# Kernel tuning notes

Hardware: AMD Instinct MI355X
Metric: run time of the kernel (lower is better)

## Reference

```python
import math
import jax, jax.numpy as jnp
import numpy as np

B, N, C = 2, 2048, 768
H, DH = 12, 64  # num_heads, head_dim


def setup_inputs() -> dict:
    key = jax.random.key(0)
    ks = jax.random.split(key, 5)
    s = 1.0 / math.sqrt(C)  # keep linear outputs O(1)
    return {
        "x": jax.random.normal(ks[0], (B, N, C), jnp.float32),
        "Wq": jax.random.normal(ks[1], (C, C), jnp.float32) * s,
        "bq": jnp.zeros((C,), jnp.float32),
        "Wk": jax.random.normal(ks[2], (C, C), jnp.float32) * s,
        "bk": jnp.zeros((C,), jnp.float32),
        "Wv": jax.random.normal(ks[3], (C, C), jnp.float32) * s,
        "bv": jnp.zeros((C,), jnp.float32),
        "Wp": jax.random.normal(ks[4], (C, C), jnp.float32) * s,
        "bp": jnp.zeros((C,), jnp.float32),
    }


def reference(x, Wq, bq, Wk, bk, Wv, bv, Wp, bp):
    # Linear projections; torch nn.Linear computes x @ W.T + b, here W stored
    # as (in, out) so it's x @ W + b with equivalent math.
    def split(t):  # [B,N,C] -> [B,H,N,DH]
        return t.reshape(B, N, H, DH).transpose(0, 2, 1, 3)

    q = split(x @ Wq + bq)
    k = split(x @ Wk + bk)
    v = split(x @ Wv + bv)
    scale = 1.0 / math.sqrt(DH)
    attn = jnp.einsum("bhqd,bhkd->bhqk", q, k) * scale  # [B,H,N,N]
    attn = jax.nn.softmax(attn, axis=-1)  # attn_drop=0.0 -> identity
    y = jnp.einsum("bhqk,bhkd->bhqd", attn, v)  # [B,H,N,DH]
    y = y.transpose(0, 2, 1, 3).reshape(B, N, C)
    return y @ Wp + bp  # proj_drop=0.0 -> identity
```

## Files before the change

### kernel.cpp

```cpp
#include <hip/hip_runtime.h>


typedef __bf16 bf16_t;
typedef __bf16 bf16x8 __attribute__((ext_vector_type(8)));
typedef __bf16 bf16x4 __attribute__((ext_vector_type(4)));
typedef short  short4_t __attribute__((ext_vector_type(4)));
typedef float  floatx4 __attribute__((ext_vector_type(4)));

#define MFMA32(a, b, c) __builtin_amdgcn_mfma_f32_16x16x32_bf16(a, b, c, 0, 0, 0)
#define MFMA16(a, b, c) __builtin_amdgcn_mfma_f32_16x16x16bf16_1k(a, b, c, 0, 0, 0)

__device__ __forceinline__ void gload16(const bf16_t* g, bf16_t* l) {
  __builtin_amdgcn_global_load_lds(
      (__attribute__((address_space(1))) void*)g,
      (__attribute__((address_space(3))) void*)l, 16, 0, 0);
}

__global__ __launch_bounds__(256) void cvt_all_kernel(
    const float* __restrict__ x, const float* __restrict__ W0,
    const float* __restrict__ W1, const float* __restrict__ W2,
    const float* __restrict__ W3, bf16_t* __restrict__ xb,
    bf16_t* __restrict__ T0, bf16_t* __restrict__ T1,
    bf16_t* __restrict__ T2, bf16_t* __restrict__ T3) {
  __shared__ bf16_t T[64][65];
  const int id = blockIdx.x;
  if (id < 3072) {
    int i = id * 256 + threadIdx.x;
    floatx4 v = ((const floatx4*)x)[i];
    bf16x4 o;
    o[0] = (bf16_t)v[0]; o[1] = (bf16_t)v[1]; o[2] = (bf16_t)v[2]; o[3] = (bf16_t)v[3];
    ((bf16x4*)xb)[i] = o;
    return;
  }
  const int wid = id - 3072;
  const int z = wid / 144, rem = wid % 144;
  const int by = rem / 12, bx = rem % 12;
  const float* W = (z == 0) ? W0 : (z == 1) ? W1 : (z == 2) ? W2 : W3;
  bf16_t* WT = (z == 0) ? T0 : (z == 1) ? T1 : (z == 2) ? T2 : T3;
  const int c = threadIdx.x & 63, r0 = threadIdx.x >> 6;
  const int i0 = by * 64, o0 = bx * 64;
#pragma unroll
  for (int p = 0; p < 16; ++p) {
    int r = p * 4 + r0;
    T[r][c] = (bf16_t)W[(i0 + r) * 768 + o0 + c];
  }
  __syncthreads();
#pragma unroll
  for (int p = 0; p < 16; ++p) {
    int r = p * 4 + r0;
    WT[(o0 + r) * 768 + i0 + c] = T[c][r];
  }
}

#define LDPG 72


#define LOADSET(KT)                                        \
  sa0 = *(const bf16x8*)(gA + (KT));                       \
  sa1 = *(const bf16x8*)(gA + (KT) + 32 * 768);            \
  sa2 = *(const bf16x8*)(gA + (KT) + 64 * 768);            \
  sa3 = *(const bf16x8*)(gA + (KT) + 96 * 768);            \
  sb0 = *(const bf16x8*)(gB + (KT));                       \
  sb1 = *(const bf16x8*)(gB + (KT) + 32 * 768);            \
  sb2 = *(const bf16x8*)(gB + (KT) + 64 * 768);            \
  sb3 = *(const bf16x8*)(gB + (KT) + 96 * 768);

#define WRITESET(LA, LB)                                   \
  *(bf16x8*)(LA) = sa0;                                    \
  *(bf16x8*)((LA) + 32 * LDPG) = sa1;                      \
  *(bf16x8*)((LA) + 64 * LDPG) = sa2;                      \
  *(bf16x8*)((LA) + 96 * LDPG) = sa3;                      \
  *(bf16x8*)(LB) = sb0;                                    \
  *(bf16x8*)((LB) + 32 * LDPG) = sb1;                      \
  *(bf16x8*)((LB) + 64 * LDPG) = sb2;                      \
  *(bf16x8*)((LB) + 96 * LDPG) = sb3;

#define GCOMPUTE(BUF)                                                       \
  {                                                                         \
    _Pragma("unroll") for (int kk2 = 0; kk2 < 2; ++kk2) {                   \
      bf16x8 af[4], bfr[4];                                                 \
      _Pragma("unroll") for (int i = 0; i < 4; ++i) {                       \
        af[i]  = *(bf16x8*)&Al[BUF][(wr * 64 + i * 16 + l15) * LDPG +       \
                                    kk2 * 32 + quad * 8];                   \
        bfr[i] = *(bf16x8*)&Bl[BUF][(wc * 64 + i * 16 + l15) * LDPG +       \
                                    kk2 * 32 + quad * 8];                   \
      }                                                                     \
      _Pragma("unroll") for (int mi = 0; mi < 4; ++mi)                      \
          _Pragma("unroll") for (int ni = 0; ni < 4; ++ni)                  \
              acc[mi][ni] = MFMA32(af[mi], bfr[ni], acc[mi][ni]);           \
    }                                                                       \
  }

#define GEMM_KLOOP()                                       \
  LOADSET(0);                                              \
  WRITESET(lA0, lB0);                                      \
  LOADSET(64);                                             \
  __syncthreads();                                         \
  for (int t = 0; t < 12; t += 2) {                        \
    GCOMPUTE(0);                                           \
    WRITESET(lA1, lB1);                      \
    if (t + 2 < 12) LOADSET((t + 2) * 64);                 \
    __syncthreads();                                       \
    GCOMPUTE(1);                                           \
    if (t + 2 < 12) {                                      \
      WRITESET(lA0, lB0);                    \
      if (t + 3 < 12) LOADSET((t + 3) * 64);               \
    }                                                      \
    __syncthreads();                                       \
  }

__global__ __launch_bounds__(256, 2) void gemm_qkv(
    const bf16_t* __restrict__ Xb, const bf16_t* __restrict__ WqT,
    const bf16_t* __restrict__ WkT, const bf16_t* __restrict__ WvT,
    const float* __restrict__ bq, const float* __restrict__ bk,
    const float* __restrict__ bv, bf16_t* __restrict__ qw,
    bf16_t* __restrict__ kw, bf16_t* __restrict__ vtw) {
  __shared__ bf16_t Al[2][128 * LDPG];
  __shared__ bf16_t Bl[2][128 * LDPG];
  const int z = blockIdx.z;
  const bf16_t* Wt = (z == 0) ? WqT : (z == 1) ? WkT : WvT;
  const float* bias = (z == 0) ? bq : (z == 1) ? bk : bv;
  const float oscale = (z == 0) ? 0.18033688011112042f : 1.0f;

  const int tid = threadIdx.x, lane = tid & 63, w = tid >> 6;
  const int wr = w >> 1, wc = w & 1;
  const int l15 = lane & 15, quad = lane >> 4;
  const int m0 = blockIdx.y * 128, n0 = blockIdx.x * 128;

  const int r0 = tid >> 3, q0c = (tid & 7) * 8;
  const bf16_t* gA = &Wt[(m0 + r0) * 768 + q0c];
  const bf16_t* gB = &Xb[(n0 + r0) * 768 + q0c];
  bf16_t* lA0 = &Al[0][r0 * LDPG + q0c];
  bf16_t* lB0 = &Bl[0][r0 * LDPG + q0c];
  bf16_t* lA1 = &Al[1][r0 * LDPG + q0c];
  bf16_t* lB1 = &Bl[1][r0 * LDPG + q0c];

  floatx4 acc[4][4] = {};
  bf16x8 sa0, sa1, sa2, sa3, sb0, sb1, sb2, sb3;

  GEMM_KLOOP();

  const int hh = (m0 + wr * 64) >> 6;
#pragma unroll
  for (int mi = 0; mi < 4; ++mi) {
    const int d0 = mi * 16 + quad * 4;
    const int gm0 = m0 + wr * 64 + d0;
    float bv4[4];
#pragma unroll
    for (int r = 0; r < 4; ++r) bv4[r] = bias[gm0 + r];
#pragma unroll
    for (int ni = 0; ni < 4; ++ni) {
      const int gn = n0 + wc * 64 + ni * 16 + l15;
      const int bb = gn >> 11, tok = gn & 2047;
      const int bh = bb * 12 + hh;
      if (z == 0) {
        bf16x4 pk;
#pragma unroll
        for (int r = 0; r < 4; ++r)
          pk[r] = (bf16_t)((acc[mi][ni][r] + bv4[r]) * oscale);
        *(bf16x4*)&qw[bh * 131072 + tok * 64 + d0] = pk;
      } else if (z == 1) {
        const int kt2 = tok >> 7, k128 = tok & 127;
        const int nk = k128 >> 4, kl15 = k128 & 15;
        const int kk = d0 >> 5, kq = (d0 >> 3) & 3, j0 = d0 & 7;
        bf16x4 pk;
#pragma unroll
        for (int r = 0; r < 4; ++r)
          pk[r] = (bf16_t)(acc[mi][ni][r] + bv4[r]);
        *(bf16x4*)&kw[bh * 131072 + kt2 * 8192 +
                      ((nk * 2 + kk) * 64 + kq * 16 + kl15) * 8 + j0] = pk;
      } else {
        const int kt2 = tok >> 7, k128 = tok & 127;
        const int nk = k128 >> 4, vq = (k128 >> 2) & 3, j = k128 & 3;
        const int nd = d0 >> 4, vl0 = d0 & 15;
        const int base = bh * 131072 + kt2 * 8192 +
                         ((nk * 4 + nd) * 64 + vq * 16 + vl0) * 4 + j;
#pragma unroll
        for (int r = 0; r < 4; ++r)
          vtw[base + r * 4] = (bf16_t)(acc[mi][ni][r] + bv4[r]);
      }
    }
  }
}

__global__ __launch_bounds__(256, 2) void gemm_proj(
    const bf16_t* __restrict__ Yb, const bf16_t* __restrict__ WpT,
    const float* __restrict__ bias, float* __restrict__ out) {
  __shared__ bf16_t Al[2][128 * LDPG];
  __shared__ bf16_t Bl[2][128 * LDPG];
  const int tid = threadIdx.x, lane = tid & 63, w = tid >> 6;
  const int wr = w >> 1, wc = w & 1;
  const int l15 = lane & 15, quad = lane >> 4;
  const int m0 = blockIdx.y * 128, n0 = blockIdx.x * 128;

  const int r0 = tid >> 3, q0c = (tid & 7) * 8;
  const bf16_t* gA = &WpT[(m0 + r0) * 768 + q0c];
  const bf16_t* gB = &Yb[(n0 + r0) * 768 + q0c];
  bf16_t* lA0 = &Al[0][r0 * LDPG + q0c];
  bf16_t* lB0 = &Bl[0][r0 * LDPG + q0c];
  bf16_t* lA1 = &Al[1][r0 * LDPG + q0c];
  bf16_t* lB1 = &Bl[1][r0 * LDPG + q0c];

  floatx4 acc[4][4] = {};
  bf16x8 sa0, sa1, sa2, sa3, sb0, sb1, sb2, sb3;

  GEMM_KLOOP();

#pragma unroll
  for (int mi = 0; mi < 4; ++mi) {
    const int gm0 = m0 + wr * 64 + mi * 16 + quad * 4;
    floatx4 bv4;
#pragma unroll
    for (int r = 0; r < 4; ++r) bv4[r] = bias[gm0 + r];
#pragma unroll
    for (int ni = 0; ni < 4; ++ni) {
      const int gn = n0 + wc * 64 + ni * 16 + l15;
      floatx4 v = acc[mi][ni] + bv4;
      *(floatx4*)&out[gn * 768 + gm0] = v;
    }
  }
}

__global__ __launch_bounds__(256, 4) void attn_kernel(
    const bf16_t* __restrict__ Q, const bf16_t* __restrict__ Kf,
    const bf16_t* __restrict__ Vf, bf16_t* __restrict__ Y) {
  __shared__ __align__(16) bf16_t smem[16384];
  __shared__ float Ls[2][2][2][16];
  float* Ox = (float*)smem;

  const int tid = threadIdx.x, lane = tid & 63, w = tid >> 6;
  const int wq = w & 1, wk = w >> 1;
  const int l15 = lane & 15, quad = lane >> 4;

  const int i = blockIdx.x;
  const int xcd = i & 7, j = i >> 3;
  const int bh = xcd * 3 + (j >> 5);
  const int q0 = (j & 31) * 64;

  const bf16_t* Qb = Q + bh * 131072;
  const bf16_t* Kg = Kf + bh * 131072 + tid * 8;
  const bf16_t* Vg = Vf + bh * 131072 + tid * 8;

  bf16x8 qf[2][2];
#pragma unroll
  for (int ni = 0; ni < 2; ++ni)
#pragma unroll
    for (int kk = 0; kk < 2; ++kk)
      qf[ni][kk] = *(const bf16x8*)&Qb[(q0 + wq * 32 + ni * 16 + l15) * 64 +
                                       kk * 32 + quad * 8];

  floatx4 oacc[2][4] = {};
  floatx4 sacc[2] = {};
  const short4_t ones = {0x3F80, 0x3F80, 0x3F80, 0x3F80};

  auto stage = [&](int b, int t) {
    const bf16_t* kg = Kg + t * 4096;
    const bf16_t* vg = Vg + t * 4096;
    bf16_t* kl = smem + b * 8192 + tid * 8;
    bf16_t* vl = smem + b * 8192 + 4096 + tid * 8;
    gload16(kg, kl);
    gload16(kg + 2048, kl + 2048);
    gload16(vg, vl);
    gload16(vg + 2048, vl + 2048);
  };

  auto compute = [&](int b) {
    const bf16_t* Kl = smem + b * 8192;
    const bf16_t* Vl = smem + b * 8192 + 4096;
    short4_t pk[2][2];
#pragma unroll
    for (int mt = 0; mt < 2; ++mt) {
      floatx4 s[2] = {};
#pragma unroll
      for (int kk = 0; kk < 2; ++kk) {
        bf16x8 kfr = *(const bf16x8*)&Kl[((wk * 2 + mt) * 2 + kk) * 512 + lane * 8];
#pragma unroll
        for (int ni = 0; ni < 2; ++ni)
          s[ni] = MFMA32(kfr, qf[ni][kk], s[ni]);
      }
#pragma unroll
      for (int ni = 0; ni < 2; ++ni) {
        bf16x4 ph;
#pragma unroll
        for (int r = 0; r < 4; ++r)
          ph[r] = (bf16_t)__builtin_amdgcn_exp2f(s[ni][r]);
        pk[mt][ni] = __builtin_bit_cast(short4_t, ph);
      }
    }
#pragma unroll
    for (int mt = 0; mt < 2; ++mt) {
#pragma unroll
      for (int nd = 0; nd < 4; ++nd) {
        bf16x4 vfr = *(const bf16x4*)&Vl[((wk * 2 + mt) * 4 + nd) * 256 + lane * 4];
        short4_t vs = __builtin_bit_cast(short4_t, vfr);
#pragma unroll
        for (int ni = 0; ni < 2; ++ni)
          oacc[ni][nd] = MFMA16(pk[mt][ni], vs, oacc[ni][nd]);
      }
#pragma unroll
      for (int ni = 0; ni < 2; ++ni)
        sacc[ni] = MFMA16(pk[mt][ni], ones, sacc[ni]);
    }
  };

  stage(0, 0);
  __syncthreads();
  for (int t = 0; t < 32; t += 2) {
    stage(1, t + 1);
    compute(0);
    __syncthreads();
    if (t + 2 < 32) stage(0, t + 2);
    compute(1);
    __syncthreads();
  }

  if (l15 == 0) {
#pragma unroll
    for (int ni = 0; ni < 2; ++ni)
#pragma unroll
      for (int r = 0; r < 4; ++r)
        Ls[wq][wk][ni][quad * 4 + r] = sacc[ni][r];
  }

#pragma unroll
  for (int ni = 0; ni < 2; ++ni)
#pragma unroll
    for (int ndl = 0; ndl < 2; ++ndl) {
      const int nd = (1 - wk) * 2 + ndl;
      *(floatx4*)&Ox[((((wq * 2 + wk) * 2 + ni) * 2 + ndl) * 64 + lane) * 4] =
          oacc[ni][nd];
    }
  __syncthreads();

  const int bb = bh / 12, h = bh % 12;
#pragma unroll
  for (int ni = 0; ni < 2; ++ni) {
    float tot[4];
#pragma unroll
    for (int r = 0; r < 4; ++r)
      tot[r] = Ls[wq][0][ni][quad * 4 + r] + Ls[wq][1][ni][quad * 4 + r];
#pragma unroll
    for (int ndl = 0; ndl < 2; ++ndl) {
      const int nd = wk * 2 + ndl;
      floatx4 o = oacc[ni][nd];
      floatx4 other =
          *(floatx4*)&Ox[((((wq * 2 + (1 - wk)) * 2 + ni) * 2 + ndl) * 64 + lane) * 4];
      o += other;
#pragma unroll
      for (int r = 0; r < 4; ++r) {
        const int tok = q0 + wq * 32 + ni * 16 + quad * 4 + r;
        const int col = h * 64 + nd * 16 + l15;
        Y[(bb * 2048 + tok) * 768 + col] = (bf16_t)(o[r] / tot[r]);
      }
    }
  }
}

extern "C" void kernel_launch(void* const* d_in, const int* in_sizes, int n_in,
                              void* d_out, int out_size, void* d_ws, size_t ws_size,
                              hipStream_t stream) {
  const float* x  = (const float*)d_in[0];
  const float* Wq = (const float*)d_in[1];
  const float* bq = (const float*)d_in[2];
  const float* Wk = (const float*)d_in[3];
  const float* bk = (const float*)d_in[4];
  const float* Wv = (const float*)d_in[5];
  const float* bv = (const float*)d_in[6];
  const float* Wp = (const float*)d_in[7];
  const float* bp = (const float*)d_in[8];
  float* out = (float*)d_out;

  char* ws = (char*)d_ws;
  bf16_t* xb  = (bf16_t*)ws; ws += (size_t)4096 * 768 * 2;
  bf16_t* WqT = (bf16_t*)ws; ws += (size_t)768 * 768 * 2;
  bf16_t* WkT = (bf16_t*)ws; ws += (size_t)768 * 768 * 2;
  bf16_t* WvT = (bf16_t*)ws; ws += (size_t)768 * 768 * 2;
  bf16_t* WpT = (bf16_t*)ws; ws += (size_t)768 * 768 * 2;
  bf16_t* qw  = (bf16_t*)ws; ws += (size_t)24 * 2048 * 64 * 2;
  bf16_t* kw  = (bf16_t*)ws; ws += (size_t)24 * 2048 * 64 * 2;
  bf16_t* vtw = (bf16_t*)ws; ws += (size_t)24 * 2048 * 64 * 2;
  bf16_t* yw  = (bf16_t*)ws; ws += (size_t)4096 * 768 * 2;

  cvt_all_kernel<<<3648, 256, 0, stream>>>(x, Wq, Wk, Wv, Wp, xb, WqT, WkT, WvT, WpT);
  gemm_qkv<<<dim3(32, 6, 3), 256, 0, stream>>>(xb, WqT, WkT, WvT, bq, bk, bv, qw, kw, vtw);
  attn_kernel<<<768, 256, 0, stream>>>(qw, kw, vtw, yw);
  gemm_proj<<<dim3(32, 6), 256, 0, stream>>>(yw, WpT, bp, out);
}
```

Before: 174.4 us.

## Split attention KV per-wave with private LDS buffers, removing block barriers

Each attention block now covers 32 queries instead of 64, and the grid doubles to 1536 blocks. The four waves each own a private slice of the key sequence and stage their own K/V tiles into per-wave LDS buffers. Because the buffers are private, the main loop synchronises with vmcnt waits rather than __syncthreads. A four-way cross-wave reduction of the output and row sums through LDS is added at the end. This trades barrier stalls for more blocks, and each block reloads Q for fewer queries, so total K/V traffic doubles.

```diff
diff --git a/kernel.cpp b/kernel.cpp
--- a/kernel.cpp
+++ b/kernel.cpp
@@ -224,29 +224,29 @@
 __global__ __launch_bounds__(256, 4) void attn_kernel(
     const bf16_t* __restrict__ Q, const bf16_t* __restrict__ Kf,
     const bf16_t* __restrict__ Vf, bf16_t* __restrict__ Y) {
-  __shared__ __align__(16) bf16_t smem[16384];
-  __shared__ float Ls[2][2][2][16];
-  float* Ox = (float*)smem;
+  __shared__ __align__(16) float E[8192];
+  __shared__ float Ls[4][2][16];
 
   const int tid = threadIdx.x, lane = tid & 63, w = tid >> 6;
-  const int wq = w & 1, wk = w >> 1;
   const int l15 = lane & 15, quad = lane >> 4;
 
   const int i = blockIdx.x;
   const int xcd = i & 7, j = i >> 3;
-  const int bh = xcd * 3 + (j >> 5);
-  const int q0 = (j & 31) * 64;
+  const int bh = xcd * 3 + (j >> 6);
+  const int q0 = (j & 63) * 32;
 
   const bf16_t* Qb = Q + bh * 131072;
-  const bf16_t* Kg = Kf + bh * 131072 + tid * 8;
-  const bf16_t* Vg = Vf + bh * 131072 + tid * 8;
+  const bf16_t* Kg = Kf + bh * 131072 + w * 1024 + lane * 8;
+  const bf16_t* Vg = Vf + bh * 131072 + w * 1024 + lane * 8;
+  bf16_t* kv = (bf16_t*)E;
+  bf16_t* kvw = kv + w * 4096 + lane * 8;
 
   bf16x8 qf[2][2];
 #pragma unroll
   for (int ni = 0; ni < 2; ++ni)
 #pragma unroll
     for (int kk = 0; kk < 2; ++kk)
-      qf[ni][kk] = *(const bf16x8*)&Qb[(q0 + wq * 32 + ni * 16 + l15) * 64 +
+      qf[ni][kk] = *(const bf16x8*)&Qb[(q0 + ni * 16 + l15) * 64 +
                                        kk * 32 + quad * 8];
 
   floatx4 oacc[2][4] = {};
@@ -256,79 +256,73 @@
   auto stage = [&](int b, int t) {
     const bf16_t* kg = Kg + t * 4096;
     const bf16_t* vg = Vg + t * 4096;
-    bf16_t* kl = smem + b * 8192 + tid * 8;
-    bf16_t* vl = smem + b * 8192 + 4096 + tid * 8;
-    gload16(kg, kl);
-    gload16(kg + 2048, kl + 2048);
-    gload16(vg, vl);
-    gload16(vg + 2048, vl + 2048);
+    bf16_t* d = kvw + b * 2048;
+    gload16(kg, d);
+    gload16(kg + 512, d + 512);
+    gload16(vg, d + 1024);
+    gload16(vg + 512, d + 1536);
   };
 
   auto compute = [&](int b) {
-    const bf16_t* Kl = smem + b * 8192;
-    const bf16_t* Vl = smem + b * 8192 + 4096;
-    short4_t pk[2][2];
-#pragma unroll
-    for (int mt = 0; mt < 2; ++mt) {
-      floatx4 s[2] = {};
+    const bf16_t* Kl = kv + w * 4096 + b * 2048;
+    const bf16_t* Vl = Kl + 1024;
+    short4_t pk[2];
+#pragma unroll
+    for (int ni = 0; ni < 2; ++ni) {
+      floatx4 s = {};
 #pragma unroll
       for (int kk = 0; kk < 2; ++kk) {
-        bf16x8 kfr = *(const bf16x8*)&Kl[((wk * 2 + mt) * 2 + kk) * 512 + lane * 8];
-#pragma unroll
-        for (int ni = 0; ni < 2; ++ni)
-          s[ni] = MFMA32(kfr, qf[ni][kk], s[ni]);
+        bf16x8 kfr = *(const bf16x8*)&Kl[kk * 512 + lane * 8];
+        s = MFMA32(kfr, qf[ni][kk], s);
       }
-#pragma unroll
-      for (int ni = 0; ni < 2; ++ni) {
-        bf16x4 ph;
-#pragma unroll
-        for (int r = 0; r < 4; ++r)
-          ph[r] = (bf16_t)__builtin_amdgcn_exp2f(s[ni][r]);
-        pk[mt][ni] = __builtin_bit_cast(short4_t, ph);
+      bf16x4 ph;
+#pragma unroll
+      for (int r = 0; r < 4; ++r)
+        ph[r] = (bf16_t)__builtin_amdgcn_exp2f(s[r]);
+      pk[ni] = __builtin_bit_cast(short4_t, ph);
+    }
+#pragma unroll
+    for (int nd = 0; nd < 4; ++nd) {
+      bf16x4 vfr = *(const bf16x4*)&Vl[nd * 256 + lane * 4];
+      short4_t vs = __builtin_bit_cast(short4_t, vfr);
+#pragma unroll
+      for (int ni = 0; ni < 2; ++ni)
+        oacc[ni][nd] = MFMA16(pk[ni], vs, oacc[ni][nd]);
+    }
+#pragma unroll
+    for (int ni = 0; ni < 2; ++ni)
+      sacc[ni] = MFMA16(pk[ni], ones, sacc[ni]);
+  };
+
+  stage(0, 0);
+  for (int t = 0; t < 31; ++t) {
+    stage((t + 1) & 1, t + 1);
+    asm volatile("s_waitcnt vmcnt(4)" ::: "memory");
+    __builtin_amdgcn_sched_barrier(0);
+    compute(t & 1);
+  }
+  asm volatile("s_waitcnt vmcnt(0)" ::: "memory");
+  __builtin_amdgcn_sched_barrier(0);
+  compute(1);
+
+  if (l15 == 0) {
+#pragma unroll
+    for (int ni = 0; ni < 2; ++ni)
+#pragma unroll
+      for (int r = 0; r < 4; ++r)
+        Ls[w][ni][quad * 4 + r] = sacc[ni][r];
+  }
+
+  __syncthreads();
+
+#pragma unroll
+  for (int ni = 0; ni < 2; ++ni)
+#pragma unroll
+    for (int nd = 0; nd < 4; ++nd) {
+      if (nd != w) {
+        const int ndl = nd - (nd > w ? 1 : 0);
+        *(floatx4*)&E[(((w * 2 + ni) * 3 + ndl) * 64 + lane) * 4] = oacc[ni][nd];
       }
-    }
-#pragma unroll
-    for (int mt = 0; mt < 2; ++mt) {
-#pragma unroll
-      for (int nd = 0; nd < 4; ++nd) {
-        bf16x4 vfr = *(const bf16x4*)&Vl[((wk * 2 + mt) * 4 + nd) * 256 + lane * 4];
-        short4_t vs = __builtin_bit_cast(short4_t, vfr);
-#pragma unroll
-        for (int ni = 0; ni < 2; ++ni)
-          oacc[ni][nd] = MFMA16(pk[mt][ni], vs, oacc[ni][nd]);
-      }
-#pragma unroll
-      for (int ni = 0; ni < 2; ++ni)
-        sacc[ni] = MFMA16(pk[mt][ni], ones, sacc[ni]);
-    }
-  };
-
-  stage(0, 0);
-  __syncthreads();
-  for (int t = 0; t < 32; t += 2) {
-    stage(1, t + 1);
-    compute(0);
-    __syncthreads();
-    if (t + 2 < 32) stage(0, t + 2);
-    compute(1);
-    __syncthreads();
-  }
-
-  if (l15 == 0) {
-#pragma unroll
-    for (int ni = 0; ni < 2; ++ni)
-#pragma unroll
-      for (int r = 0; r < 4; ++r)
-        Ls[wq][wk][ni][quad * 4 + r] = sacc[ni][r];
-  }
-
-#pragma unroll
-  for (int ni = 0; ni < 2; ++ni)
-#pragma unroll
-    for (int ndl = 0; ndl < 2; ++ndl) {
-      const int nd = (1 - wk) * 2 + ndl;
-      *(floatx4*)&Ox[((((wq * 2 + wk) * 2 + ni) * 2 + ndl) * 64 + lane) * 4] =
-          oacc[ni][nd];
     }
   __syncthreads();
 
@@ -338,20 +332,24 @@
     float tot[4];
 #pragma unroll
     for (int r = 0; r < 4; ++r)
-      tot[r] = Ls[wq][0][ni][quad * 4 + r] + Ls[wq][1][ni][quad * 4 + r];
-#pragma unroll
-    for (int ndl = 0; ndl < 2; ++ndl) {
-      const int nd = wk * 2 + ndl;
-      floatx4 o = oacc[ni][nd];
-      floatx4 other =
-          *(floatx4*)&Ox[((((wq * 2 + (1 - wk)) * 2 + ni) * 2 + ndl) * 64 + lane) * 4];
-      o += other;
-#pragma unroll
-      for (int r = 0; r < 4; ++r) {
-        const int tok = q0 + wq * 32 + ni * 16 + quad * 4 + r;
-        const int col = h * 64 + nd * 16 + l15;
-        Y[(bb * 2048 + tok) * 768 + col] = (bf16_t)(o[r] / tot[r]);
+      tot[r] = Ls[0][ni][quad * 4 + r] + Ls[1][ni][quad * 4 + r] +
+               Ls[2][ni][quad * 4 + r] + Ls[3][ni][quad * 4 + r];
+    floatx4 o = (w == 0) ? oacc[ni][0]
+              : (w == 1) ? oacc[ni][1]
+              : (w == 2) ? oacc[ni][2]
+                         : oacc[ni][3];
+#pragma unroll
+    for (int s = 0; s < 4; ++s) {
+      if (s != w) {
+        const int ndl = w - (w > s ? 1 : 0);
+        o += *(const floatx4*)&E[(((s * 2 + ni) * 3 + ndl) * 64 + lane) * 4];
       }
+    }
+#pragma unroll
+    for (int r = 0; r < 4; ++r) {
+      const int tok = q0 + ni * 16 + quad * 4 + r;
+      const int col = h * 64 + w * 16 + l15;
+      Y[(bb * 2048 + tok) * 768 + col] = (bf16_t)(o[r] / tot[r]);
     }
   }
 }
@@ -383,6 +381,6 @@
 
   cvt_all_kernel<<<3648, 256, 0, stream>>>(x, Wq, Wk, Wv, Wp, xb, WqT, WkT, WvT, WpT);
   gemm_qkv<<<dim3(32, 6, 3), 256, 0, stream>>>(xb, WqT, WkT, WvT, bq, bk, bv, qw, kw, vtw);
-  attn_kernel<<<768, 256, 0, stream>>>(qw, kw, vtw, yw);
+  attn_kernel<<<1536, 256, 0, stream>>>(qw, kw, vtw, yw);
   gemm_proj<<<dim3(32, 6), 256, 0, stream>>>(yw, WpT, bp, out);
 }
```

Measured after the change: 175.0 us. About the same (+0.3%).
